# Optimization experiments

Hardware: AMD Instinct MI355X
Metric: run time of the kernel (lower is better)

The kernel has to match this reference:

```python
import jax, jax.numpy as jnp
import numpy as np

D_MODEL = 1024
N_HEADS = 16
D_KEYS = D_MODEL // N_HEADS


def setup_inputs() -> dict:
    key = jax.random.key(0)
    ks = jax.random.split(key, 11)
    B, L, S = 2, 2048, 2048
    inp = {
        "queries": jax.random.normal(ks[0], (B, L, D_MODEL), dtype=jnp.float32),
        "keys": jax.random.normal(ks[1], (B, S, D_MODEL), dtype=jnp.float32),
        "values": jax.random.normal(ks[2], (B, S, D_MODEL), dtype=jnp.float32),
        # Linear params, scaled like torch default init (~U(-1/sqrt(D), 1/sqrt(D)))
        "Wq": jax.random.normal(ks[3], (D_MODEL, D_MODEL), dtype=jnp.float32) / np.sqrt(D_MODEL),
        "bq": jax.random.normal(ks[4], (D_MODEL,), dtype=jnp.float32) / np.sqrt(D_MODEL),
        "Wk": jax.random.normal(ks[5], (D_MODEL, D_MODEL), dtype=jnp.float32) / np.sqrt(D_MODEL),
        "bk": jax.random.normal(ks[6], (D_MODEL,), dtype=jnp.float32) / np.sqrt(D_MODEL),
        "Wv": jax.random.normal(ks[7], (D_MODEL, D_MODEL), dtype=jnp.float32) / np.sqrt(D_MODEL),
        "bv": jax.random.normal(ks[8], (D_MODEL,), dtype=jnp.float32) / np.sqrt(D_MODEL),
        "Wo": jax.random.normal(ks[9], (D_MODEL, D_MODEL), dtype=jnp.float32) / np.sqrt(D_MODEL),
        "bo": jax.random.normal(ks[10], (D_MODEL,), dtype=jnp.float32) / np.sqrt(D_MODEL),
    }
    return inp


def reference(queries, keys, values, Wq, bq, Wk, bk, Wv, bv, Wo, bo):
    B, L, _ = queries.shape
    S = keys.shape[1]
    H, E = N_HEADS, D_KEYS
    scale = E ** (-0.5)
    q = (queries @ Wq.T + bq).reshape(B, L, H, E)
    k = (keys @ Wk.T + bk).reshape(B, S, H, E)
    v = (values @ Wv.T + bv).reshape(B, S, H, E)
    scores = jnp.einsum('blhe,bshe->bhls', q, k)
    attn = jax.nn.softmax(scores * scale, axis=-1)  # dropout = identity in eval
    out = jnp.einsum('bhls,bshe->blhe', attn, v).reshape(B, L, H * E)
    return out @ Wo.T + bo
```

## Files before the change

### kernel.cpp

```cpp
#include <hip/hip_runtime.h>

typedef unsigned short u16;
typedef unsigned int u32;
typedef __attribute__((ext_vector_type(8))) short short8;
typedef __attribute__((ext_vector_type(4))) short s16x4;
typedef __attribute__((ext_vector_type(4))) float f32x4;
typedef __attribute__((ext_vector_type(16))) float f32x16;

#define DEVI __device__ __forceinline__

#define LSEQ 2048
#define DMODEL 1024
#define NH 16
#define EHD 64

#define QSCALE 0.18033688011112042f

#if __has_builtin(__builtin_amdgcn_exp2f)
#define EXP2(x) __builtin_amdgcn_exp2f(x)
#else
#define EXP2(x) exp2f(x)
#endif

DEVI u16 f2b(float f) {
    u32 u = __float_as_uint(f);
    return (u16)((u + 0x7FFFu + ((u >> 16) & 1u)) >> 16);
}

DEVI u32 cvtpk(float lo, float hi) {
    u32 r;
    asm("v_cvt_pk_bf16_f32 %0, %1, %2" : "=v"(r) : "v"(lo), "v"(hi));
    return r;
}

DEVI void swap32(u32& a, u32& b) {
    asm("v_permlane32_swap_b32 %0, %1" : "+v"(a), "+v"(b));
}

DEVI short8 mk8(u32 a0, u32 a1, u32 a2, u32 a3) {
    union { u32 u[4]; short8 s; } x;
    x.u[0] = a0; x.u[1] = a1; x.u[2] = a2; x.u[3] = a3;
    return x.s;
}

DEVI void async_cp16(const u16* g, u16* l) {
    __builtin_amdgcn_global_load_lds((const __attribute__((address_space(1))) u32*)g,
                                     (__attribute__((address_space(3))) u32*)l, 16, 0, 0);
}

DEVI short8 lds_swz(const u16* base, int row, int colb) {
    int off = (row << 7) + (colb ^ ((row & 7) << 4));
    return *(const short8*)((const char*)base + off);
}

__global__ __launch_bounds__(256) void cvt_all(const float* __restrict__ q,
                                               const float* __restrict__ k,
                                               const float* __restrict__ v,
                                               const float* __restrict__ wq,
                                               const float* __restrict__ wk,
                                               const float* __restrict__ wv,
                                               const float* __restrict__ wo,
                                               u16* __restrict__ dst) {
    const size_t NX8 = (size_t)2 * LSEQ * DMODEL / 8;
    const size_t NW8 = (size_t)DMODEL * DMODEL / 8;
    int bid = blockIdx.x;
    const float* src;
    size_t base;
    int rel;
    if (bid < 2048)      { src = q;  base = 0;             rel = bid; }
    else if (bid < 4096) { src = k;  base = NX8;           rel = bid - 2048; }
    else if (bid < 6144) { src = v;  base = 2 * NX8;       rel = bid - 4096; }
    else if (bid < 6656) { src = wq; base = 3 * NX8;             rel = bid - 6144; }
    else if (bid < 7168) { src = wk; base = 3 * NX8 + NW8;       rel = bid - 6656; }
    else if (bid < 7680) { src = wv; base = 3 * NX8 + 2 * NW8;   rel = bid - 7168; }
    else                 { src = wo; base = 3 * NX8 + 3 * NW8;   rel = bid - 7680; }
    size_t i = (size_t)rel * 256 + threadIdx.x;
    const float4* p = (const float4*)(src + i * 8);
    float4 a = p[0], c = p[1];
    short8 o;
    o[0] = (short)f2b(a.x); o[1] = (short)f2b(a.y);
    o[2] = (short)f2b(a.z); o[3] = (short)f2b(a.w);
    o[4] = (short)f2b(c.x); o[5] = (short)f2b(c.y);
    o[6] = (short)f2b(c.z); o[7] = (short)f2b(c.w);
    *(short8*)(dst + (base + i) * 8) = o;
}

__global__ __launch_bounds__(256) void gemm_qkv(const u16* __restrict__ X,
                                                const u16* __restrict__ W3,
                                                const float* __restrict__ bq,
                                                const float* __restrict__ bk,
                                                const float* __restrict__ bv,
                                                u16* __restrict__ Qp,
                                                u16* __restrict__ Kp,
                                                u16* __restrict__ Vt) {
    __shared__ __align__(16) u16 As[3][4096];
    __shared__ __align__(16) u16 Bs[3][4096];
    const int tid = threadIdx.x;
    const int lane = tid & 63, w = tid >> 6;
    const int lr = lane & 15, lk = lane >> 4;
    const int wr = w >> 1, wc = w & 1;
    const int bid = blockIdx.x;
    const int xcd = bid & 7, rr = bid >> 3;
    const int rb = (xcd * 4 + rr / 24) * 128;
    const int xtile = rr % 24;
    const int cb = xtile * 128;
    const int K = DMODEL;
    const int seg = xtile >> 3;
    const u16* A = X + (size_t)seg * ((size_t)2 * LSEQ * DMODEL);

    f32x4 acc[4][4] = {};

    const int arow = lane >> 2;
    const int acol = (lane & 3) * 8;

#define QKV_STAGE(bb, kk)                                                           \
    do {                                                                            \
        _Pragma("unroll") for (int c2 = 0; c2 < 2; ++c2) {                          \
            int c = w * 2 + c2;                                                     \
            async_cp16(A + (size_t)(rb + c * 16 + arow) * K + (kk) + acol,          \
                       &As[bb][c * 512]);                                           \
            async_cp16(W3 + (size_t)(cb + c * 16 + arow) * K + (kk) + acol,         \
                       &Bs[bb][c * 512]);                                           \
        }                                                                           \
    } while (0)

#define QKV_ITER(bc, bs, tt)                                                          \
    do {                                                                              \
        if ((tt) + 2 < 32) QKV_STAGE(bs, ((tt) + 2) * 32);                            \
        short8 af[4], bfr[4];                                                         \
        _Pragma("unroll") for (int m = 0; m < 4; m++)                                 \
            af[m] = *(const short8*)(&As[bc][(wr * 64 + m * 16 + lr) * 32 + lk * 8]); \
        _Pragma("unroll") for (int n = 0; n < 4; n++)                                 \
            bfr[n] = *(const short8*)(&Bs[bc][(wc * 64 + n * 16 + lr) * 32 + lk * 8]); \
        __builtin_amdgcn_s_setprio(1);                                                \
        _Pragma("unroll") for (int m = 0; m < 4; m++)                                 \
            _Pragma("unroll") for (int n = 0; n < 4; n++)                             \
                acc[m][n] =                                                           \
                    __builtin_amdgcn_mfma_f32_16x16x32_bf16(af[m], bfr[n], acc[m][n], 0, 0, 0); \
        __builtin_amdgcn_s_setprio(0);                                                \
        if ((tt) + 2 < 32) asm volatile("s_waitcnt vmcnt(4)" ::: "memory");           \
        else               asm volatile("s_waitcnt vmcnt(0)" ::: "memory");           \
        __builtin_amdgcn_s_barrier();                                                 \
    } while (0)

    QKV_STAGE(0, 0);
    QKV_STAGE(1, 32);
    asm volatile("s_waitcnt vmcnt(4)" ::: "memory");
    __builtin_amdgcn_s_barrier();

    for (int tb = 0; tb < 30; tb += 3) {
        QKV_ITER(0, 2, tb);
        QKV_ITER(1, 0, tb + 1);
        QKV_ITER(2, 1, tb + 2);
    }
    QKV_ITER(0, 2, 30);
    QKV_ITER(1, 0, 31);

    const float* bp = seg == 0 ? bq : (seg == 1 ? bk : bv);
    const float sc = seg == 0 ? QSCALE : 1.0f;

#pragma unroll
    for (int n = 0; n < 4; n++) {
        int col = cb + wc * 64 + n * 16 + lr;
        int c2 = col & 1023;
        float bvv = bp[c2];
#pragma unroll
        for (int m = 0; m < 4; m++) {
            int row0 = rb + wr * 64 + m * 16 + lk * 4;
            if (seg == 2) {
                s16x4 pk4;
#pragma unroll
                for (int r = 0; r < 4; r++) pk4[r] = (short)f2b(acc[m][n][r] + bvv);
                size_t idx = (((size_t)(row0 >> 11) * NH + (c2 >> 6)) * EHD + (c2 & 63)) * LSEQ +
                             (row0 & (LSEQ - 1));
                *(s16x4*)(Vt + idx) = pk4;
            } else {
                u16* dst = seg == 0 ? Qp : Kp;
#pragma unroll
                for (int r = 0; r < 4; r++)
                    dst[(size_t)(row0 + r) * DMODEL + c2] = f2b((acc[m][n][r] + bvv) * sc);
            }
        }
    }
}

__global__ __launch_bounds__(256) void gemm_out(const u16* __restrict__ A,
                                                const u16* __restrict__ B,
                                                const float* __restrict__ bias,
                                                float* __restrict__ C) {
    __shared__ __align__(16) u16 As[3][4096];
    __shared__ __align__(16) u16 Bs[3][2048];
    const int tid = threadIdx.x;
    const int lane = tid & 63, w = tid >> 6;
    const int lr = lane & 15, lk = lane >> 4;
    const int wr = w >> 1, wc = w & 1;
    const int bid = blockIdx.x;
    const int xcd = bid & 7, rr = bid >> 3;
    const int rb = (xcd * 4 + rr / 16) * 128;
    const int cb = (rr % 16) * 64;
    const int K = DMODEL, N = DMODEL;

    f32x4 acc[4][2] = {};

    const int arow = lane >> 2;
    const int acol = (lane & 3) * 8;

#define OUT_STAGE(bb, kk)                                                           \
    do {                                                                            \
        _Pragma("unroll") for (int c2 = 0; c2 < 2; ++c2) {                          \
            int c = w * 2 + c2;                                                     \
            async_cp16(A + (size_t)(rb + c * 16 + arow) * K + (kk) + acol,          \
                       &As[bb][c * 512]);                                           \
        }                                                                           \
        async_cp16(B + (size_t)(cb + w * 16 + arow) * K + (kk) + acol,              \
                   &Bs[bb][w * 512]);                                               \
    } while (0)

#define OUT_ITER(bc, bs, tt)                                                          \
    do {                                                                              \
        if ((tt) + 2 < 32) OUT_STAGE(bs, ((tt) + 2) * 32);                            \
        short8 af[4], bfr[2];                                                         \
        _Pragma("unroll") for (int m = 0; m < 4; m++)                                 \
            af[m] = *(const short8*)(&As[bc][(wr * 64 + m * 16 + lr) * 32 + lk * 8]); \
        _Pragma("unroll") for (int n = 0; n < 2; n++)                                 \
            bfr[n] = *(const short8*)(&Bs[bc][(wc * 32 + n * 16 + lr) * 32 + lk * 8]); \
        __builtin_amdgcn_s_setprio(1);                                                \
        _Pragma("unroll") for (int m = 0; m < 4; m++)                                 \
            _Pragma("unroll") for (int n = 0; n < 2; n++)                             \
                acc[m][n] =                                                           \
                    __builtin_amdgcn_mfma_f32_16x16x32_bf16(af[m], bfr[n], acc[m][n], 0, 0, 0); \
        __builtin_amdgcn_s_setprio(0);                                                \
        if ((tt) + 2 < 32) asm volatile("s_waitcnt vmcnt(3)" ::: "memory");           \
        else               asm volatile("s_waitcnt vmcnt(0)" ::: "memory");           \
        __builtin_amdgcn_s_barrier();                                                 \
    } while (0)

    OUT_STAGE(0, 0);
    OUT_STAGE(1, 32);
    asm volatile("s_waitcnt vmcnt(3)" ::: "memory");
    __builtin_amdgcn_s_barrier();

    for (int tb = 0; tb < 30; tb += 3) {
        OUT_ITER(0, 2, tb);
        OUT_ITER(1, 0, tb + 1);
        OUT_ITER(2, 1, tb + 2);
    }
    OUT_ITER(0, 2, 30);
    OUT_ITER(1, 0, 31);

#pragma unroll
    for (int n = 0; n < 2; n++) {
        int col = cb + wc * 32 + n * 16 + lr;
        float bv = bias[col];
#pragma unroll
        for (int m = 0; m < 4; m++) {
            int row0 = rb + wr * 64 + m * 16 + lk * 4;
#pragma unroll
            for (int r = 0; r < 4; r++)
                C[(size_t)(row0 + r) * N + col] = acc[m][n][r] + bv;
        }
    }
}

__global__ __launch_bounds__(512) void attn_kernel(const u16* __restrict__ Q,
                                                   const u16* __restrict__ Kp,
                                                   const u16* __restrict__ Vtb,
                                                   u16* __restrict__ Hid) {
    const int bid = blockIdx.x;
    const int j = bid >> 3;
    const int bh = (bid & 7) + 8 * (j >> 3);
    const int q0 = (j & 7) * 256;
    const int b = bh >> 4, h = bh & 15;
    const int tid = threadIdx.x, lane = tid & 63, w = tid >> 6;
    const int l31 = lane & 31, hi = lane >> 5;
    const int qb = q0 + w * 32;

    __shared__ __align__(16) u16 Ks[2][8192];
    __shared__ __align__(16) u16 Vs[2][2][4096];

    short8 qf[4];
#pragma unroll
    for (int eg = 0; eg < 4; eg++)
        qf[eg] = *(const short8*)(Q + (size_t)(b * LSEQ + qb + l31) * DMODEL + h * EHD +
                                  eg * 16 + hi * 8);

    const int trow = tid >> 3;
    const int slot = tid & 7;
    const int swz8 = ((slot ^ (trow & 7)) * 8);
    size_t kbase[2], vbase[2];
#pragma unroll
    for (int jj = 0; jj < 2; jj++) {
        kbase[jj] = (size_t)(b * LSEQ + jj * 64 + trow) * DMODEL + h * EHD + swz8;
        vbase[jj] = ((size_t)bh * EHD + trow) * LSEQ + jj * 64 + swz8;
    }

#define ATTN_STAGE(bb, s0v)                                                           \
    do {                                                                              \
        async_cp16(Kp + kbase[0] + (size_t)(s0v)*DMODEL, &Ks[bb][w * 512]);           \
        async_cp16(Kp + kbase[1] + (size_t)(s0v)*DMODEL, &Ks[bb][4096 + w * 512]);    \
        async_cp16(Vtb + vbase[0] + (s0v), &Vs[bb][0][w * 512]);                      \
        async_cp16(Vtb + vbase[1] + (s0v), &Vs[bb][1][w * 512]);                      \
    } while (0)

    f32x16 o0 = (f32x16)0.f, o1 = (f32x16)0.f, lsum = (f32x16)0.f;
    const u32 one2 = 0x3F803F80u;
    const short8 ones = mk8(one2, one2, one2, one2);

    ATTN_STAGE(0, 0);
    asm volatile("s_waitcnt vmcnt(0)" ::: "memory");
    __syncthreads();

    int cur = 0;
    for (int t = 0; t < LSEQ / 128; ++t) {
        if (t + 1 < LSEQ / 128) ATTN_STAGE(cur ^ 1, (t + 1) * 128);

#pragma unroll
        for (int hf = 0; hf < 2; hf++) {
            f32x16 s0 = (f32x16)0.f, s1 = (f32x16)0.f;
            __builtin_amdgcn_s_setprio(1);
#pragma unroll
            for (int eg = 0; eg < 4; eg++) {
                short8 kf0 = lds_swz(&Ks[cur][0], hf * 64 + l31, eg * 32 + hi * 16);
                short8 kf1 = lds_swz(&Ks[cur][0], hf * 64 + 32 + l31, eg * 32 + hi * 16);
                s0 = __builtin_amdgcn_mfma_f32_32x32x16_bf16(kf0, qf[eg], s0, 0, 0, 0);
                s1 = __builtin_amdgcn_mfma_f32_32x32x16_bf16(kf1, qf[eg], s1, 0, 0, 0);
            }
            __builtin_amdgcn_s_setprio(0);

#pragma unroll
            for (int r = 0; r < 16; r++) {
                s0[r] = EXP2(s0[r]);
                s1[r] = EXP2(s1[r]);
            }

            short8 paf[4];
#pragma unroll
            for (int kc = 0; kc < 4; kc++) {
                int ro = (kc & 1) * 8;
                u32 u0, u1, u2, u3;
                if (kc < 2) {
                    u0 = cvtpk(s0[ro + 0], s0[ro + 1]); u1 = cvtpk(s0[ro + 2], s0[ro + 3]);
                    u2 = cvtpk(s0[ro + 4], s0[ro + 5]); u3 = cvtpk(s0[ro + 6], s0[ro + 7]);
                } else {
                    u0 = cvtpk(s1[ro + 0], s1[ro + 1]); u1 = cvtpk(s1[ro + 2], s1[ro + 3]);
                    u2 = cvtpk(s1[ro + 4], s1[ro + 5]); u3 = cvtpk(s1[ro + 6], s1[ro + 7]);
                }
                swap32(u0, u2);
                swap32(u1, u3);
                paf[kc] = mk8(u0, u1, u2, u3);
            }

            __builtin_amdgcn_s_setprio(1);
#pragma unroll
            for (int kc = 0; kc < 4; kc++) {
                short8 vf0 = lds_swz(&Vs[cur][hf][0], l31, kc * 32 + hi * 16);
                short8 vf1 = lds_swz(&Vs[cur][hf][0], 32 + l31, kc * 32 + hi * 16);
                o0 = __builtin_amdgcn_mfma_f32_32x32x16_bf16(paf[kc], vf0, o0, 0, 0, 0);
                o1 = __builtin_amdgcn_mfma_f32_32x32x16_bf16(paf[kc], vf1, o1, 0, 0, 0);
                lsum = __builtin_amdgcn_mfma_f32_32x32x16_bf16(paf[kc], ones, lsum, 0, 0, 0);
            }
            __builtin_amdgcn_s_setprio(0);
        }

        asm volatile("s_waitcnt vmcnt(0)" ::: "memory");
        __syncthreads();
        cur ^= 1;
    }

#pragma unroll
    for (int r = 0; r < 16; r++) {
        float li = 1.0f / lsum[r];
        int qrow = qb + (r & 3) + 8 * (r >> 2) + 4 * hi;
        size_t base = (size_t)(b * LSEQ + qrow) * DMODEL + h * EHD;
        Hid[base + l31] = f2b(o0[r] * li);
        Hid[base + 32 + l31] = f2b(o1[r] * li);
    }
}

extern "C" void kernel_launch(void* const* d_in, const int* in_sizes, int n_in,
                              void* d_out, int out_size, void* d_ws, size_t ws_size,
                              hipStream_t stream) {
    const float* queries = (const float*)d_in[0];
    const float* keys    = (const float*)d_in[1];
    const float* values  = (const float*)d_in[2];
    const float* Wq = (const float*)d_in[3];
    const float* bq = (const float*)d_in[4];
    const float* Wk = (const float*)d_in[5];
    const float* bk = (const float*)d_in[6];
    const float* Wv = (const float*)d_in[7];
    const float* bv = (const float*)d_in[8];
    const float* Wo = (const float*)d_in[9];
    const float* bo = (const float*)d_in[10];
    float* out = (float*)d_out;

    const size_t NX = (size_t)2 * LSEQ * DMODEL;
    const size_t NW = (size_t)DMODEL * DMODEL;

    u16* p = (u16*)d_ws;
    u16* Xq = p;  p += NX;
    u16* Xk = p;  p += NX;
    u16* Xv = p;  p += NX;
    u16* Wqb = p; p += NW;
    u16* Wkb = p; p += NW;
    u16* Wvb = p; p += NW;
    u16* Wob = p; p += NW;
    u16* Qp = p;  p += NX;
    u16* Kp = p;  p += NX;
    u16* Vt = p;  p += NX;
    u16* Hid = p; p += NX;
    (void)Xk; (void)Xv; (void)Wkb; (void)Wvb;

    cvt_all<<<8192, 256, 0, stream>>>(queries, keys, values, Wq, Wk, Wv, Wo, Xq);

    gemm_qkv<<<768, 256, 0, stream>>>(Xq, Wqb, bq, bk, bv, Qp, Kp, Vt);

    attn_kernel<<<256, 512, 0, stream>>>(Qp, Kp, Vt, Hid);

    gemm_out<<<512, 256, 0, stream>>>(Hid, Wob, bo, out);
}
```

Measured before the change: 130.7 us.

## Fuse fp32-to-bf16 activation conversion into QKV GEMM loads

The separate conversion pass over the query, key and value activations is removed. The QKV GEMM now streams fp32 activations straight into swizzled LDS and converts them to bf16 while building fragments, so only the weights are still pre-converted. This drops a full write and re-read of the bf16 activation copies. In exchange the A tile doubles in LDS size, the pipeline drops from triple to double buffering with full vmcnt(0) waits each iteration, and conversion instructions are added to the GEMM inner loop.

```diff
diff --git a/kernel.cpp b/kernel.cpp
--- a/kernel.cpp
+++ b/kernel.cpp
@@ -43,7 +43,7 @@
     return x.s;
 }
 
-DEVI void async_cp16(const u16* g, u16* l) {
+DEVI void async_cp16(const void* g, void* l) {
     __builtin_amdgcn_global_load_lds((const __attribute__((address_space(1))) u32*)g,
                                      (__attribute__((address_space(3))) u32*)l, 16, 0, 0);
 }
@@ -53,27 +53,24 @@
     return *(const short8*)((const char*)base + off);
 }
 
-__global__ __launch_bounds__(256) void cvt_all(const float* __restrict__ q,
-                                               const float* __restrict__ k,
-                                               const float* __restrict__ v,
-                                               const float* __restrict__ wq,
-                                               const float* __restrict__ wk,
-                                               const float* __restrict__ wv,
-                                               const float* __restrict__ wo,
-                                               u16* __restrict__ dst) {
-    const size_t NX8 = (size_t)2 * LSEQ * DMODEL / 8;
-    const size_t NW8 = (size_t)DMODEL * DMODEL / 8;
+DEVI short8 lds_a_frag(const float* base, int row, int lk) {
+    int s0 = (2 * lk) ^ (row & 7);
+    int s1 = (2 * lk + 1) ^ (row & 7);
+    f32x4 lo = *(const f32x4*)(base + row * 32 + s0 * 4);
+    f32x4 hi = *(const f32x4*)(base + row * 32 + s1 * 4);
+    return mk8(cvtpk(lo[0], lo[1]), cvtpk(lo[2], lo[3]),
+               cvtpk(hi[0], hi[1]), cvtpk(hi[2], hi[3]));
+}
+
+__global__ __launch_bounds__(256) void cvt_w(const float* __restrict__ wq,
+                                             const float* __restrict__ wk,
+                                             const float* __restrict__ wv,
+                                             const float* __restrict__ wo,
+                                             u16* __restrict__ dst) {
     int bid = blockIdx.x;
-    const float* src;
-    size_t base;
-    int rel;
-    if (bid < 2048)      { src = q;  base = 0;             rel = bid; }
-    else if (bid < 4096) { src = k;  base = NX8;           rel = bid - 2048; }
-    else if (bid < 6144) { src = v;  base = 2 * NX8;       rel = bid - 4096; }
-    else if (bid < 6656) { src = wq; base = 3 * NX8;             rel = bid - 6144; }
-    else if (bid < 7168) { src = wk; base = 3 * NX8 + NW8;       rel = bid - 6656; }
-    else if (bid < 7680) { src = wv; base = 3 * NX8 + 2 * NW8;   rel = bid - 7168; }
-    else                 { src = wo; base = 3 * NX8 + 3 * NW8;   rel = bid - 7680; }
+    const float* src = bid < 512 ? wq : (bid < 1024 ? wk : (bid < 1536 ? wv : wo));
+    int rel = bid & 511;
+    size_t base = (size_t)(bid >> 9) * ((size_t)DMODEL * DMODEL);
     size_t i = (size_t)rel * 256 + threadIdx.x;
     const float4* p = (const float4*)(src + i * 8);
     float4 a = p[0], c = p[1];
@@ -82,10 +79,12 @@
     o[2] = (short)f2b(a.z); o[3] = (short)f2b(a.w);
     o[4] = (short)f2b(c.x); o[5] = (short)f2b(c.y);
     o[6] = (short)f2b(c.z); o[7] = (short)f2b(c.w);
-    *(short8*)(dst + (base + i) * 8) = o;
-}
-
-__global__ __launch_bounds__(256) void gemm_qkv(const u16* __restrict__ X,
+    *(short8*)(dst + base + i * 8) = o;
+}
+
+__global__ __launch_bounds__(256) void gemm_qkv(const float* __restrict__ Xq,
+                                                const float* __restrict__ Xk,
+                                                const float* __restrict__ Xv,
                                                 const u16* __restrict__ W3,
                                                 const float* __restrict__ bq,
                                                 const float* __restrict__ bk,
@@ -93,8 +92,8 @@
                                                 u16* __restrict__ Qp,
                                                 u16* __restrict__ Kp,
                                                 u16* __restrict__ Vt) {
-    __shared__ __align__(16) u16 As[3][4096];
-    __shared__ __align__(16) u16 Bs[3][4096];
+    __shared__ __align__(16) float Af[2][4096];
+    __shared__ __align__(16) u16 Bs[2][4096];
     const int tid = threadIdx.x;
     const int lane = tid & 63, w = tid >> 6;
     const int lr = lane & 15, lk = lane >> 4;
@@ -106,55 +105,58 @@
     const int cb = xtile * 128;
     const int K = DMODEL;
     const int seg = xtile >> 3;
-    const u16* A = X + (size_t)seg * ((size_t)2 * LSEQ * DMODEL);
+    const float* A = seg == 0 ? Xq : (seg == 1 ? Xk : Xv);
 
     f32x4 acc[4][4] = {};
 
     const int arow = lane >> 2;
     const int acol = (lane & 3) * 8;
 
-#define QKV_STAGE(bb, kk)                                                           \
-    do {                                                                            \
-        _Pragma("unroll") for (int c2 = 0; c2 < 2; ++c2) {                          \
-            int c = w * 2 + c2;                                                     \
-            async_cp16(A + (size_t)(rb + c * 16 + arow) * K + (kk) + acol,          \
-                       &As[bb][c * 512]);                                           \
-            async_cp16(W3 + (size_t)(cb + c * 16 + arow) * K + (kk) + acol,         \
-                       &Bs[bb][c * 512]);                                           \
-        }                                                                           \
+    const float* Aptr[4];
+#pragma unroll
+    for (int i = 0; i < 4; ++i) {
+        int row = (i * 4 + w) * 8 + (lane >> 3);
+        Aptr[i] = A + (size_t)(rb + row) * K + (((lane & 7) ^ (row & 7)) * 4);
+    }
+
+#define QKV_STAGE(bb, kk)                                                            \
+    do {                                                                             \
+        _Pragma("unroll") for (int i = 0; i < 4; ++i)                                \
+            async_cp16(Aptr[i] + (kk), &Af[bb][(i * 4 + w) * 256]);                  \
+        _Pragma("unroll") for (int c2 = 0; c2 < 2; ++c2) {                           \
+            int c = w * 2 + c2;                                                      \
+            async_cp16(W3 + (size_t)(cb + c * 16 + arow) * K + (kk) + acol,          \
+                       &Bs[bb][c * 512]);                                            \
+        }                                                                            \
     } while (0)
 
-#define QKV_ITER(bc, bs, tt)                                                          \
-    do {                                                                              \
-        if ((tt) + 2 < 32) QKV_STAGE(bs, ((tt) + 2) * 32);                            \
-        short8 af[4], bfr[4];                                                         \
-        _Pragma("unroll") for (int m = 0; m < 4; m++)                                 \
-            af[m] = *(const short8*)(&As[bc][(wr * 64 + m * 16 + lr) * 32 + lk * 8]); \
-        _Pragma("unroll") for (int n = 0; n < 4; n++)                                 \
-            bfr[n] = *(const short8*)(&Bs[bc][(wc * 64 + n * 16 + lr) * 32 + lk * 8]); \
-        __builtin_amdgcn_s_setprio(1);                                                \
-        _Pragma("unroll") for (int m = 0; m < 4; m++)                                 \
-            _Pragma("unroll") for (int n = 0; n < 4; n++)                             \
-                acc[m][n] =                                                           \
-                    __builtin_amdgcn_mfma_f32_16x16x32_bf16(af[m], bfr[n], acc[m][n], 0, 0, 0); \
-        __builtin_amdgcn_s_setprio(0);                                                \
-        if ((tt) + 2 < 32) asm volatile("s_waitcnt vmcnt(4)" ::: "memory");           \
-        else               asm volatile("s_waitcnt vmcnt(0)" ::: "memory");           \
-        __builtin_amdgcn_s_barrier();                                                 \
-    } while (0)
-
     QKV_STAGE(0, 0);
-    QKV_STAGE(1, 32);
-    asm volatile("s_waitcnt vmcnt(4)" ::: "memory");
-    __builtin_amdgcn_s_barrier();
-
-    for (int tb = 0; tb < 30; tb += 3) {
-        QKV_ITER(0, 2, tb);
-        QKV_ITER(1, 0, tb + 1);
-        QKV_ITER(2, 1, tb + 2);
-    }
-    QKV_ITER(0, 2, 30);
-    QKV_ITER(1, 0, 31);
+    asm volatile("s_waitcnt vmcnt(0)" ::: "memory");
+    __syncthreads();
+
+    int cur = 0;
+    for (int k0 = 0; k0 < K; k0 += 32) {
+        if (k0 + 32 < K) QKV_STAGE(cur ^ 1, k0 + 32);
+
+        short8 af[4], bfr[4];
+#pragma unroll
+        for (int m = 0; m < 4; m++)
+            af[m] = lds_a_frag(&Af[cur][0], wr * 64 + m * 16 + lr, lk);
+#pragma unroll
+        for (int n = 0; n < 4; n++)
+            bfr[n] = *(const short8*)(&Bs[cur][(wc * 64 + n * 16 + lr) * 32 + lk * 8]);
+        __builtin_amdgcn_s_setprio(1);
+#pragma unroll
+        for (int m = 0; m < 4; m++)
+#pragma unroll
+            for (int n = 0; n < 4; n++)
+                acc[m][n] = __builtin_amdgcn_mfma_f32_16x16x32_bf16(af[m], bfr[n], acc[m][n], 0, 0, 0);
+        __builtin_amdgcn_s_setprio(0);
+
+        asm volatile("s_waitcnt vmcnt(0)" ::: "memory");
+        __syncthreads();
+        cur ^= 1;
+    }
 
     const float* bp = seg == 0 ? bq : (seg == 1 ? bk : bv);
     const float sc = seg == 0 ? QSCALE : 1.0f;
@@ -397,9 +399,6 @@
     const size_t NW = (size_t)DMODEL * DMODEL;
 
     u16* p = (u16*)d_ws;
-    u16* Xq = p;  p += NX;
-    u16* Xk = p;  p += NX;
-    u16* Xv = p;  p += NX;
     u16* Wqb = p; p += NW;
     u16* Wkb = p; p += NW;
     u16* Wvb = p; p += NW;
@@ -408,11 +407,11 @@
     u16* Kp = p;  p += NX;
     u16* Vt = p;  p += NX;
     u16* Hid = p; p += NX;
-    (void)Xk; (void)Xv; (void)Wkb; (void)Wvb;
-
-    cvt_all<<<8192, 256, 0, stream>>>(queries, keys, values, Wq, Wk, Wv, Wo, Xq);
-
-    gemm_qkv<<<768, 256, 0, stream>>>(Xq, Wqb, bq, bk, bv, Qp, Kp, Vt);
+    (void)Wkb; (void)Wvb;
+
+    cvt_w<<<2048, 256, 0, stream>>>(Wq, Wk, Wv, Wo, Wqb);
+
+    gemm_qkv<<<768, 256, 0, stream>>>(queries, keys, values, Wqb, bq, bk, bv, Qp, Kp, Vt);
 
     attn_kernel<<<256, 512, 0, stream>>>(Qp, Kp, Vt, Hid);
 
```

Measured after the change: 134.8 us. 3.2% more time.

## Shrink QKV GEMM tile to 128x64 with double buffering for more blocks

Applied to the files above, without the earlier changes.

The QKV projection GEMM now uses 128x64 output tiles instead of 128x128, doubling the grid to 1536 blocks. The triple-buffered, hand-unrolled pipeline becomes a simpler double-buffered loop that waits on all loads each iteration, and launch bounds now request 5 blocks per SM. The aim is better occupancy and load balance across CUs. In exchange, each block reuses fewer operands, the A tile is fetched twice as often, and the full vmcnt(0) wait gives less overlap between loads and compute.

```diff
diff --git a/kernel.cpp b/kernel.cpp
--- a/kernel.cpp
+++ b/kernel.cpp
@@ -43,7 +43,7 @@
     return x.s;
 }
 
-DEVI void async_cp16(const u16* g, u16* l) {
+DEVI void async_cp16(const void* g, void* l) {
     __builtin_amdgcn_global_load_lds((const __attribute__((address_space(1))) u32*)g,
                                      (__attribute__((address_space(3))) u32*)l, 16, 0, 0);
 }
@@ -85,83 +85,75 @@
     *(short8*)(dst + (base + i) * 8) = o;
 }
 
-__global__ __launch_bounds__(256) void gemm_qkv(const u16* __restrict__ X,
-                                                const u16* __restrict__ W3,
-                                                const float* __restrict__ bq,
-                                                const float* __restrict__ bk,
-                                                const float* __restrict__ bv,
-                                                u16* __restrict__ Qp,
-                                                u16* __restrict__ Kp,
-                                                u16* __restrict__ Vt) {
-    __shared__ __align__(16) u16 As[3][4096];
-    __shared__ __align__(16) u16 Bs[3][4096];
+__global__ __launch_bounds__(256, 5) void gemm_qkv(const u16* __restrict__ X,
+                                                   const u16* __restrict__ W3,
+                                                   const float* __restrict__ bq,
+                                                   const float* __restrict__ bk,
+                                                   const float* __restrict__ bv,
+                                                   u16* __restrict__ Qp,
+                                                   u16* __restrict__ Kp,
+                                                   u16* __restrict__ Vt) {
+    __shared__ __align__(16) u16 As[2][4096];
+    __shared__ __align__(16) u16 Bs[2][2048];
     const int tid = threadIdx.x;
     const int lane = tid & 63, w = tid >> 6;
     const int lr = lane & 15, lk = lane >> 4;
     const int wr = w >> 1, wc = w & 1;
     const int bid = blockIdx.x;
     const int xcd = bid & 7, rr = bid >> 3;
-    const int rb = (xcd * 4 + rr / 24) * 128;
-    const int xtile = rr % 24;
-    const int cb = xtile * 128;
+    const int rb = (xcd * 4 + rr / 48) * 128;
+    const int xtile = rr % 48;
+    const int cb = xtile * 64;
     const int K = DMODEL;
-    const int seg = xtile >> 3;
+    const int seg = xtile >> 4;
     const u16* A = X + (size_t)seg * ((size_t)2 * LSEQ * DMODEL);
 
-    f32x4 acc[4][4] = {};
-
-    const int arow = lane >> 2;
-    const int acol = (lane & 3) * 8;
-
-#define QKV_STAGE(bb, kk)                                                           \
-    do {                                                                            \
-        _Pragma("unroll") for (int c2 = 0; c2 < 2; ++c2) {                          \
-            int c = w * 2 + c2;                                                     \
-            async_cp16(A + (size_t)(rb + c * 16 + arow) * K + (kk) + acol,          \
-                       &As[bb][c * 512]);                                           \
-            async_cp16(W3 + (size_t)(cb + c * 16 + arow) * K + (kk) + acol,         \
-                       &Bs[bb][c * 512]);                                           \
-        }                                                                           \
+    f32x4 acc[4][2] = {};
+
+    const int sra = tid >> 2, ska = (tid & 3) * 8;
+
+#define QKV_STAGE(bb, kk)                                                            \
+    do {                                                                             \
+        async_cp16(A + (size_t)(rb + sra) * K + (kk) + ska, &As[bb][tid * 8]);       \
+        async_cp16(A + (size_t)(rb + 64 + sra) * K + (kk) + ska,                     \
+                   &As[bb][2048 + tid * 8]);                                         \
+        async_cp16(W3 + (size_t)(cb + sra) * K + (kk) + ska, &Bs[bb][tid * 8]);      \
     } while (0)
 
-#define QKV_ITER(bc, bs, tt)                                                          \
-    do {                                                                              \
-        if ((tt) + 2 < 32) QKV_STAGE(bs, ((tt) + 2) * 32);                            \
-        short8 af[4], bfr[4];                                                         \
-        _Pragma("unroll") for (int m = 0; m < 4; m++)                                 \
-            af[m] = *(const short8*)(&As[bc][(wr * 64 + m * 16 + lr) * 32 + lk * 8]); \
-        _Pragma("unroll") for (int n = 0; n < 4; n++)                                 \
-            bfr[n] = *(const short8*)(&Bs[bc][(wc * 64 + n * 16 + lr) * 32 + lk * 8]); \
-        __builtin_amdgcn_s_setprio(1);                                                \
-        _Pragma("unroll") for (int m = 0; m < 4; m++)                                 \
-            _Pragma("unroll") for (int n = 0; n < 4; n++)                             \
-                acc[m][n] =                                                           \
-                    __builtin_amdgcn_mfma_f32_16x16x32_bf16(af[m], bfr[n], acc[m][n], 0, 0, 0); \
-        __builtin_amdgcn_s_setprio(0);                                                \
-        if ((tt) + 2 < 32) asm volatile("s_waitcnt vmcnt(4)" ::: "memory");           \
-        else               asm volatile("s_waitcnt vmcnt(0)" ::: "memory");           \
-        __builtin_amdgcn_s_barrier();                                                 \
-    } while (0)
-
     QKV_STAGE(0, 0);
-    QKV_STAGE(1, 32);
-    asm volatile("s_waitcnt vmcnt(4)" ::: "memory");
-    __builtin_amdgcn_s_barrier();
-
-    for (int tb = 0; tb < 30; tb += 3) {
-        QKV_ITER(0, 2, tb);
-        QKV_ITER(1, 0, tb + 1);
-        QKV_ITER(2, 1, tb + 2);
-    }
-    QKV_ITER(0, 2, 30);
-    QKV_ITER(1, 0, 31);
+    asm volatile("s_waitcnt vmcnt(0)" ::: "memory");
+    __syncthreads();
+
+    int cur = 0;
+    for (int k0 = 0; k0 < K; k0 += 32) {
+        if (k0 + 32 < K) QKV_STAGE(cur ^ 1, k0 + 32);
+
+        short8 af[4], bfr[2];
+#pragma unroll
+        for (int m = 0; m < 4; m++)
+            af[m] = *(const short8*)(&As[cur][(wr * 64 + m * 16 + lr) * 32 + lk * 8]);
+#pragma unroll
+        for (int n = 0; n < 2; n++)
+            bfr[n] = *(const short8*)(&Bs[cur][(wc * 32 + n * 16 + lr) * 32 + lk * 8]);
+        __builtin_amdgcn_s_setprio(1);
+#pragma unroll
+        for (int m = 0; m < 4; m++)
+#pragma unroll
+            for (int n = 0; n < 2; n++)
+                acc[m][n] = __builtin_amdgcn_mfma_f32_16x16x32_bf16(af[m], bfr[n], acc[m][n], 0, 0, 0);
+        __builtin_amdgcn_s_setprio(0);
+
+        asm volatile("s_waitcnt vmcnt(0)" ::: "memory");
+        __syncthreads();
+        cur ^= 1;
+    }
 
     const float* bp = seg == 0 ? bq : (seg == 1 ? bk : bv);
     const float sc = seg == 0 ? QSCALE : 1.0f;
 
 #pragma unroll
-    for (int n = 0; n < 4; n++) {
-        int col = cb + wc * 64 + n * 16 + lr;
+    for (int n = 0; n < 2; n++) {
+        int col = cb + wc * 32 + n * 16 + lr;
         int c2 = col & 1023;
         float bvv = bp[c2];
 #pragma unroll
@@ -412,7 +404,7 @@
 
     cvt_all<<<8192, 256, 0, stream>>>(queries, keys, values, Wq, Wk, Wv, Wo, Xq);
 
-    gemm_qkv<<<768, 256, 0, stream>>>(Xq, Wqb, bq, bk, bv, Qp, Kp, Vt);
+    gemm_qkv<<<1536, 256, 0, stream>>>(Xq, Wqb, bq, bk, bv, Qp, Kp, Vt);
 
     attn_kernel<<<256, 512, 0, stream>>>(Qp, Kp, Vt, Hid);
 
```

Result: no change. 131.6 us (+0.7%).
